# Kernel tuning notes

Hardware: AMD Instinct MI355X
Metric: run time of the kernel (lower is better)

## Reference

```python
import jax, jax.numpy as jnp
import numpy as np

B, U, D, SKIP = 2048, 1024, 1024, 24

def setup_inputs() -> dict:
    key = jax.random.key(0)
    ks = jax.random.split(key, 8)
    return {
        "inputs": jax.random.normal(ks[0], (B, D), dtype=jnp.float32),
        "h_tm1": jax.random.normal(ks[1], (B, 4 * U), dtype=jnp.float32),
        "c_tm1": jax.random.normal(ks[2], (B, U), dtype=jnp.float32),
        "step": jnp.zeros((B, 1), dtype=jnp.float32),
        "prev_h": jax.random.normal(ks[3], (B, U * SKIP), dtype=jnp.float32),
        "kernel": jax.random.normal(ks[4], (D, 4 * U), dtype=jnp.float32) * (1.0 / np.sqrt(D)),
        "recurrent_kernel": jax.random.normal(ks[5], (U, 4 * U), dtype=jnp.float32) * (1.0 / np.sqrt(U)),
        "kernel2": jax.random.normal(ks[6], (U, U), dtype=jnp.float32) * (1.0 / np.sqrt(U)),
        "bias": jnp.zeros((4 * U,), dtype=jnp.float32),
        "bias2": jnp.zeros((U,), dtype=jnp.float32),
        "s0": jnp.float32(0.5),
    }

def reference(inputs, h_tm1, c_tm1, step, prev_h, kernel, recurrent_kernel, kernel2, bias, bias2, s0):
    units = kernel2.shape[0]
    # split previous 'h' state into its four gate-history blocks [B, U] each
    h_parts = jnp.stack(jnp.split(h_tm1, 4, axis=1), axis=0)          # [4, B, U]
    rk = recurrent_kernel.reshape(units, 4, units)                     # [U, 4, U]
    # fused per-gate recurrent matmuls: r[g] = h_parts[g] @ recurrent_kernel[:, g*U:(g+1)*U]
    r = jnp.einsum('gbu,ugv->gbv', h_parts, rk)                        # [4, B, U]
    x = inputs @ kernel + bias                                         # [B, 4U]
    x_i, x_f, x_c, x_o = jnp.split(x, 4, axis=1)
    i = jax.nn.sigmoid(x_i + r[0])
    f = jax.nn.sigmoid(x_f + r[1])
    c = f * c_tm1 + i * jnp.tanh(x_c + r[2])
    o = jax.nn.sigmoid(x_o + r[3])
    h = o * jnp.tanh(c)
    new_h_skip = jax.nn.sigmoid(prev_h[:, :units] @ kernel2 + bias2)
    h = s0 * h + new_h_skip * (1 - s0)
    new_h_tm1 = jnp.concatenate([i, f, c, o], axis=1)
    new_prev_h = jnp.concatenate([prev_h[:, units:], h], axis=1)
    return (h, new_h_tm1, c, step + 1, new_prev_h)
```

## Files before the change

### kernel.cpp

```cpp
#include <hip/hip_runtime.h>
#include <hip/hip_bf16.h>
#include <stdint.h>

#define BB 2048
#define UU 1024
#define SKIPN 24

typedef __attribute__((ext_vector_type(8))) short short8;
typedef __attribute__((ext_vector_type(4))) float f32x4;
typedef __attribute__((ext_vector_type(4))) unsigned short ushort4_t;

static __device__ __forceinline__ float sigmoidf_(float x) {
    return 1.0f / (1.0f + __expf(-x));
}

static __device__ __forceinline__ void load_lds16(const void* g, void* l) {
    __builtin_amdgcn_global_load_lds((const __attribute__((address_space(1))) void*)g,
                                     (__attribute__((address_space(3))) void*)l, 16, 0, 0);
}

static __device__ __forceinline__ f32x4 ntl(const f32x4* p) {
    return __builtin_nontemporal_load(p);
}
static __device__ __forceinline__ void nts(f32x4* p, f32x4 v) {
    __builtin_nontemporal_store(v, p);
}

__global__ __launch_bounds__(256) void prep(
    const float* __restrict__ inputs, const float* __restrict__ h_tm1,
    const float* __restrict__ prev_h, const float* __restrict__ kernel,
    const float* __restrict__ rkernel, const float* __restrict__ kernel2,
    __hip_bfloat16* __restrict__ kt, __hip_bfloat16* __restrict__ rkt,
    __hip_bfloat16* __restrict__ k2t, __hip_bfloat16* __restrict__ xin,
    __hip_bfloat16* __restrict__ hb, __hip_bfloat16* __restrict__ ph0) {
    const int bid = blockIdx.x;
    if (bid < 9216) {
        __shared__ float tile[32][33];
        const float* src;
        __hip_bfloat16* dst;
        int C, local;
        if (bid < 4096)      { src = kernel;  dst = kt;  C = 4096; local = bid; }
        else if (bid < 8192) { src = rkernel; dst = rkt; C = 4096; local = bid - 4096; }
        else                 { src = kernel2; dst = k2t; C = 1024; local = bid - 8192; }
        const int xt = (C == 4096) ? 128 : 32;
        const int bc = (local % xt) * 32;
        const int br = (local / xt) * 32;
        const int tx = threadIdx.x & 31, ty = threadIdx.x >> 5;
#pragma unroll
        for (int i = 0; i < 32; i += 8)
            tile[ty + i][tx] = src[(size_t)(br + ty + i) * C + bc + tx];
        __syncthreads();
#pragma unroll
        for (int i = 0; i < 32; i += 8)
            dst[(size_t)(bc + ty + i) * 1024 + br + tx] = __float2bfloat16(tile[tx][ty + i]);
    } else {
        const int idx = (bid - 9216) * 256 + threadIdx.x;
        const float* src;
        __hip_bfloat16* dst;
        int off;
        if (idx < 524288) { dst = xin; off = idx; src = inputs + (size_t)off * 4; }
        else if (idx < 2621440) { off = idx - 524288; dst = hb; src = h_tm1 + (size_t)off * 4; }
        else {
            const int i = idx - 2621440;
            const int b = i >> 8, c4 = i & 255;
            off = i; dst = ph0;
            src = prev_h + (size_t)b * (UU * SKIPN) + c4 * 4;
        }
        const float4 v = *(const float4*)src;
        union { __hip_bfloat16 h[4]; ushort4_t u; } cv;
        cv.h[0] = __float2bfloat16(v.x);
        cv.h[1] = __float2bfloat16(v.y);
        cv.h[2] = __float2bfloat16(v.z);
        cv.h[3] = __float2bfloat16(v.w);
        *(ushort4_t*)(dst + (size_t)off * 4) = cv.u;
    }
}

__global__ __launch_bounds__(256) void mega4(
    const __hip_bfloat16* __restrict__ xin,
    const __hip_bfloat16* __restrict__ hb,
    const __hip_bfloat16* __restrict__ ph0,
    const __hip_bfloat16* __restrict__ kt,
    const __hip_bfloat16* __restrict__ rkt,
    const __hip_bfloat16* __restrict__ k2t,
    const float* __restrict__ prev_h, float* __restrict__ out_prev,
    float* __restrict__ pre) {
    const int bid = blockIdx.x;
    if (bid >= 640) {
        const int b = bid - 640;
        const f32x4* s = (const f32x4*)(prev_h + (size_t)b * 24576 + 1024);
        f32x4* d = (f32x4*)(out_prev + (size_t)b * 24576);
        int c = threadIdx.x;
#pragma unroll 1
        for (int it = 0; it < 5; ++it) {
            f32x4 v0 = ntl(s + c);
            f32x4 v1 = ntl(s + c + 256);
            f32x4 v2 = ntl(s + c + 512);
            f32x4 v3 = ntl(s + c + 768);
            nts(d + c, v0);
            nts(d + c + 256, v1);
            nts(d + c + 512, v2);
            nts(d + c + 768, v3);
            c += 1024;
        }
        {
            f32x4 v0 = ntl(s + c);
            f32x4 v1 = ntl(s + c + 256);
            f32x4 v2 = ntl(s + c + 512);
            nts(d + c, v0);
            nts(d + c + 256, v1);
            nts(d + c + 512, v2);
        }
        return;
    }
    const int gi = bid;
    const int g = gi % 5;
    const int t = gi / 5;
    const int v0 = (t & 7) * 128;
    const int b0 = (t >> 3) * 128;

    __shared__ char As[2 * 8192];
    __shared__ char Bs[2 * 8192];

    const int tid = threadIdx.x;
    const int lane = tid & 63;
    const int wid = tid >> 6;
    const int wrow = wid >> 1;
    const int wcol = wid & 1;

    const int srow = tid >> 2;
    const int sslot = tid & 3;
    const int kofs = ((sslot ^ (srow & 3)) << 3);
    const int ldst = wid * 1024;

    const int l15 = lane & 15;
    const int hi = lane >> 4;
    const int rswB = ((hi ^ (l15 & 3)) << 4);

    f32x4 acc[4][4];
#pragma unroll
    for (int m = 0; m < 4; m++)
#pragma unroll
        for (int n = 0; n < 4; n++) acc[m][n] = (f32x4){0.f, 0.f, 0.f, 0.f};

    const __hip_bfloat16* A1;
    const __hip_bfloat16* W1;
    const __hip_bfloat16* A2 = nullptr;
    const __hip_bfloat16* W2 = nullptr;
    int lda1;
    if (g < 4) {
        A1 = xin; lda1 = 1024;
        W1 = kt + (size_t)g * 1048576;
        A2 = hb + (size_t)g * 1024;
        W2 = rkt + (size_t)g * 1048576;
    } else {
        A1 = ph0; lda1 = 1024;
        W1 = k2t;
    }

#define BARRIER() asm volatile("s_barrier" ::: "memory")
#define WAITV(N) asm volatile("s_waitcnt vmcnt(" #N ")" ::: "memory")
#define WAITL0() asm volatile("s_waitcnt lgkmcnt(0)" ::: "memory")

#define KSEG(AB, LDA, WB)                                                          \
    {                                                                              \
        const __hip_bfloat16* Ar0 = (AB) + (size_t)(b0 + srow) * (LDA) + kofs;     \
        const __hip_bfloat16* Ar1 = (AB) + (size_t)(b0 + 64 + srow) * (LDA) + kofs;\
        const __hip_bfloat16* Wr0 = (WB) + (size_t)(v0 + srow) * 1024 + kofs;      \
        const __hip_bfloat16* Wr1 = (WB) + (size_t)(v0 + 64 + srow) * 1024 + kofs; \
        load_lds16(Ar0, As + ldst);                                                \
        load_lds16(Ar1, As + ldst + 4096);                                         \
        load_lds16(Wr0, Bs + ldst);                                                \
        load_lds16(Wr1, Bs + ldst + 4096);                                         \
        _Pragma("unroll 2")                                                        \
        for (int t_ = 0; t_ < 32; ++t_) {                                          \
            const int cur = t_ & 1;                                                \
            char* Ac = As + cur * 8192;                                            \
            char* Bc = Bs + cur * 8192;                                            \
            if (t_ < 31) {                                                         \
                const int kn = (t_ + 1) * 32;                                      \
                char* An = As + (cur ^ 1) * 8192 + ldst;                           \
                char* Bn = Bs + (cur ^ 1) * 8192 + ldst;                           \
                load_lds16(Ar0 + kn, An);                                          \
                load_lds16(Ar1 + kn, An + 4096);                                   \
                load_lds16(Wr0 + kn, Bn);                                          \
                load_lds16(Wr1 + kn, Bn + 4096);                                   \
                WAITV(4);                                                          \
            } else {                                                               \
                WAITV(0);                                                          \
            }                                                                      \
            BARRIER();                                                             \
            short8 af[4], bfr[4];                                                  \
            _Pragma("unroll")                                                      \
            for (int m = 0; m < 4; m++)                                            \
                af[m] = *(const short8*)(Ac + (wrow * 64 + m * 16 + l15) * 64 + rswB); \
            _Pragma("unroll")                                                      \
            for (int n = 0; n < 4; n++)                                            \
                bfr[n] = *(const short8*)(Bc + (wcol * 64 + n * 16 + l15) * 64 + rswB); \
            _Pragma("unroll")                                                      \
            for (int m = 0; m < 4; m++)                                            \
                _Pragma("unroll")                                                  \
                for (int n = 0; n < 4; n++)                                        \
                    acc[m][n] = __builtin_amdgcn_mfma_f32_16x16x32_bf16(af[m], bfr[n], acc[m][n], 0, 0, 0); \
            WAITL0();                                                              \
            BARRIER();                                                             \
        }                                                                          \
    }

    KSEG(A1, lda1, W1);
    if (g < 4) KSEG(A2, 4096, W2);
#undef KSEG

    float* P = pre + (size_t)g * 2097152;
#pragma unroll
    for (int m = 0; m < 4; m++) {
#pragma unroll
        for (int n = 0; n < 4; n++) {
            const int col = v0 + wcol * 64 + n * 16 + l15;
            const int row = b0 + wrow * 64 + m * 16 + hi * 4;
#pragma unroll
            for (int r = 0; r < 4; r++)
                P[(size_t)(row + r) * 1024 + col] = acc[m][n][r];
        }
    }
#undef BARRIER
#undef WAITV
#undef WAITL0
}

__global__ __launch_bounds__(256) void epilogue2(
    const float* __restrict__ pre,
    const float* __restrict__ c_tm1, const float* __restrict__ bias,
    const float* __restrict__ bias2, const float* __restrict__ s0p,
    const float* __restrict__ step, float* __restrict__ out_h,
    float* __restrict__ out_ht, float* __restrict__ out_c,
    float* __restrict__ out_step, float* __restrict__ out_prev, int write_tail) {
    const int idx = blockIdx.x * 256 + threadIdx.x;
    const int b = idx >> 8;
    const int v = (idx & 255) * 4;
    const size_t bv = (size_t)b * 1024 + v;
    const float4 pi = *(const float4*)(pre + bv);
    const float4 pf = *(const float4*)(pre + 2097152 + bv);
    const float4 pc = *(const float4*)(pre + 4194304 + bv);
    const float4 po = *(const float4*)(pre + 6291456 + bv);
    const float4 ps = *(const float4*)(pre + 8388608 + bv);
    const float4 ct = *(const float4*)(c_tm1 + bv);
    const float4 bi = *(const float4*)(bias + v);
    const float4 bf_ = *(const float4*)(bias + 1024 + v);
    const float4 bc = *(const float4*)(bias + 2048 + v);
    const float4 bo = *(const float4*)(bias + 3072 + v);
    const float4 b2 = *(const float4*)(bias2 + v);
    const float s0 = s0p[0];

    float4 hv, iv4, fv4, cn4, ov4;
#pragma unroll
    for (int j = 0; j < 4; j++) {
        const float iv = sigmoidf_(((const float*)&pi)[j] + ((const float*)&bi)[j]);
        const float fv = sigmoidf_(((const float*)&pf)[j] + ((const float*)&bf_)[j]);
        const float cn = fv * ((const float*)&ct)[j] + iv * tanhf(((const float*)&pc)[j] + ((const float*)&bc)[j]);
        const float ov = sigmoidf_(((const float*)&po)[j] + ((const float*)&bo)[j]);
        const float sk = sigmoidf_(((const float*)&ps)[j] + ((const float*)&b2)[j]);
        ((float*)&hv)[j] = s0 * (ov * tanhf(cn)) + sk * (1.0f - s0);
        ((float*)&iv4)[j] = iv;
        ((float*)&fv4)[j] = fv;
        ((float*)&cn4)[j] = cn;
        ((float*)&ov4)[j] = ov;
    }
    *(float4*)(out_h + bv) = hv;
    *(float4*)(out_c + bv) = cn4;
    float* ht = out_ht + (size_t)b * 4096 + v;
    *(float4*)(ht) = iv4;
    *(float4*)(ht + 1024) = fv4;
    *(float4*)(ht + 2048) = cn4;
    *(float4*)(ht + 3072) = ov4;
    if (write_tail)
        *(float4*)(out_prev + (size_t)b * 24576 + 23552 + v) = hv;
    if (idx < 2048) out_step[idx] = step[idx] + 1.0f;
}

__global__ __launch_bounds__(256) void shift_only(
    const float* __restrict__ prev_h, const float* __restrict__ out_h,
    float* __restrict__ out_prev) {
    const int b = blockIdx.x;
    float4* d = (float4*)(out_prev + (size_t)b * 24576);
    const float4* s1 = (const float4*)(prev_h + (size_t)b * 24576 + 1024);
    const float4* s2 = (const float4*)(out_h + (size_t)b * 1024);
    for (int c = threadIdx.x; c < 6144; c += 256)
        d[c] = (c < 5888) ? s1[c] : s2[c - 5888];
}

extern "C" void kernel_launch(void* const* d_in, const int* in_sizes, int n_in,
                              void* d_out, int out_size, void* d_ws, size_t ws_size,
                              hipStream_t stream) {
    (void)in_sizes; (void)n_in; (void)out_size;
    const float* inputs = (const float*)d_in[0];
    const float* h_tm1 = (const float*)d_in[1];
    const float* c_tm1 = (const float*)d_in[2];
    const float* step = (const float*)d_in[3];
    const float* prev_h = (const float*)d_in[4];
    const float* kernel = (const float*)d_in[5];
    const float* rkernel = (const float*)d_in[6];
    const float* kernel2 = (const float*)d_in[7];
    const float* bias = (const float*)d_in[8];
    const float* bias2 = (const float*)d_in[9];
    const float* s0 = (const float*)d_in[10];

    float* out = (float*)d_out;
    float* out_h = out;
    float* out_ht = out + 2097152;
    float* out_c = out + 10485760;
    float* out_step = out + 12582912;
    float* out_prev = out + 12584960;

    const size_t NEED = 44040192 + 41943040;
    const int fits = (ws_size >= NEED);
    char* scr = fits ? (char*)d_ws : (char*)out_prev;
    __hip_bfloat16* kt = (__hip_bfloat16*)(scr + 0);
    __hip_bfloat16* rkt = (__hip_bfloat16*)(scr + 8388608);
    __hip_bfloat16* k2t = (__hip_bfloat16*)(scr + 16777216);
    __hip_bfloat16* xin = (__hip_bfloat16*)(scr + 18874368);
    __hip_bfloat16* hb = (__hip_bfloat16*)(scr + 23068672);
    __hip_bfloat16* ph0 = (__hip_bfloat16*)(scr + 39845888);
    float* pre = (float*)(scr + 44040192);

    prep<<<21504, 256, 0, stream>>>(inputs, h_tm1, prev_h, kernel, rkernel, kernel2,
                                    kt, rkt, k2t, xin, hb, ph0);
    if (fits) {
        mega4<<<2688, 256, 0, stream>>>(xin, hb, ph0, kt, rkt, k2t, prev_h, out_prev, pre);
        epilogue2<<<2048, 256, 0, stream>>>(pre, c_tm1, bias, bias2, s0, step,
                                            out_h, out_ht, out_c, out_step, out_prev, 1);
    } else {
        mega4<<<640, 256, 0, stream>>>(xin, hb, ph0, kt, rkt, k2t, prev_h, out_prev, pre);
        epilogue2<<<2048, 256, 0, stream>>>(pre, c_tm1, bias, bias2, s0, step,
                                            out_h, out_ht, out_c, out_step, out_prev, 0);
        shift_only<<<2048, 256, 0, stream>>>(prev_h, out_h, out_prev);
    }
}
```

Baseline: 173.8 us.

## Triple-buffer GEMM LDS pipeline and store preactivations in bf16

Moves the GEMM k-loop from double to triple buffering in LDS, prefetching two k-tiles ahead to hide more global-load latency. Stores the intermediate preactivation buffer as bf16 instead of fp32, halving its write and read traffic and the workspace requirement. The epilogue is reworked to handle 8 elements per thread with half as many blocks. The bf16 rounding of preactivations adds precision loss, and the extra LDS per block may reduce occupancy.

```diff
diff --git a/kernel.cpp b/kernel.cpp
--- a/kernel.cpp
+++ b/kernel.cpp
@@ -76,7 +76,7 @@
     }
 }
 
-__global__ __launch_bounds__(256) void mega4(
+__global__ __launch_bounds__(256) void mega5(
     const __hip_bfloat16* __restrict__ xin,
     const __hip_bfloat16* __restrict__ hb,
     const __hip_bfloat16* __restrict__ ph0,
@@ -84,7 +84,7 @@
     const __hip_bfloat16* __restrict__ rkt,
     const __hip_bfloat16* __restrict__ k2t,
     const float* __restrict__ prev_h, float* __restrict__ out_prev,
-    float* __restrict__ pre) {
+    __hip_bfloat16* __restrict__ pre) {
     const int bid = blockIdx.x;
     if (bid >= 640) {
         const int b = bid - 640;
@@ -119,8 +119,8 @@
     const int v0 = (t & 7) * 128;
     const int b0 = (t >> 3) * 128;
 
-    __shared__ char As[2 * 8192];
-    __shared__ char Bs[2 * 8192];
+    __shared__ char As[3 * 8192];
+    __shared__ char Bs[3 * 8192];
 
     const int tid = threadIdx.x;
     const int lane = tid & 63;
@@ -172,19 +172,25 @@
         load_lds16(Ar1, As + ldst + 4096);                                         \
         load_lds16(Wr0, Bs + ldst);                                                \
         load_lds16(Wr1, Bs + ldst + 4096);                                         \
-        _Pragma("unroll 2")                                                        \
+        load_lds16(Ar0 + 32, As + 8192 + ldst);                                    \
+        load_lds16(Ar1 + 32, As + 8192 + ldst + 4096);                             \
+        load_lds16(Wr0 + 32, Bs + 8192 + ldst);                                    \
+        load_lds16(Wr1 + 32, Bs + 8192 + ldst + 4096);                             \
+        int cur = 0;                                                               \
         for (int t_ = 0; t_ < 32; ++t_) {                                          \
-            const int cur = t_ & 1;                                                \
             char* Ac = As + cur * 8192;                                            \
             char* Bc = Bs + cur * 8192;                                            \
-            if (t_ < 31) {                                                         \
-                const int kn = (t_ + 1) * 32;                                      \
-                char* An = As + (cur ^ 1) * 8192 + ldst;                           \
-                char* Bn = Bs + (cur ^ 1) * 8192 + ldst;                           \
+            if (t_ < 30) {                                                         \
+                int nxt = cur + 2; if (nxt >= 3) nxt -= 3;                         \
+                const int kn = (t_ + 2) * 32;                                      \
+                char* An = As + nxt * 8192 + ldst;                                 \
+                char* Bn = Bs + nxt * 8192 + ldst;                                 \
                 load_lds16(Ar0 + kn, An);                                          \
                 load_lds16(Ar1 + kn, An + 4096);                                   \
                 load_lds16(Wr0 + kn, Bn);                                          \
                 load_lds16(Wr1 + kn, Bn + 4096);                                   \
+                WAITV(8);                                                          \
+            } else if (t_ == 30) {                                                 \
                 WAITV(4);                                                          \
             } else {                                                               \
                 WAITV(0);                                                          \
@@ -204,6 +210,7 @@
                     acc[m][n] = __builtin_amdgcn_mfma_f32_16x16x32_bf16(af[m], bfr[n], acc[m][n], 0, 0, 0); \
             WAITL0();                                                              \
             BARRIER();                                                             \
+            cur = (cur == 2) ? 0 : cur + 1;                                        \
         }                                                                          \
     }
 
@@ -211,7 +218,7 @@
     if (g < 4) KSEG(A2, 4096, W2);
 #undef KSEG
 
-    float* P = pre + (size_t)g * 2097152;
+    __hip_bfloat16* P = pre + (size_t)g * 2097152;
 #pragma unroll
     for (int m = 0; m < 4; m++) {
 #pragma unroll
@@ -220,7 +227,7 @@
             const int row = b0 + wrow * 64 + m * 16 + hi * 4;
 #pragma unroll
             for (int r = 0; r < 4; r++)
-                P[(size_t)(row + r) * 1024 + col] = acc[m][n][r];
+                P[(size_t)(row + r) * 1024 + col] = __float2bfloat16(acc[m][n][r]);
         }
     }
 #undef BARRIER
@@ -228,53 +235,61 @@
 #undef WAITL0
 }
 
-__global__ __launch_bounds__(256) void epilogue2(
-    const float* __restrict__ pre,
+__global__ __launch_bounds__(256) void epilogue3(
+    const __hip_bfloat16* __restrict__ pre,
     const float* __restrict__ c_tm1, const float* __restrict__ bias,
     const float* __restrict__ bias2, const float* __restrict__ s0p,
     const float* __restrict__ step, float* __restrict__ out_h,
     float* __restrict__ out_ht, float* __restrict__ out_c,
     float* __restrict__ out_step, float* __restrict__ out_prev, int write_tail) {
     const int idx = blockIdx.x * 256 + threadIdx.x;
-    const int b = idx >> 8;
-    const int v = (idx & 255) * 4;
+    const int b = idx >> 7;
+    const int v = (idx & 127) * 8;
     const size_t bv = (size_t)b * 1024 + v;
-    const float4 pi = *(const float4*)(pre + bv);
-    const float4 pf = *(const float4*)(pre + 2097152 + bv);
-    const float4 pc = *(const float4*)(pre + 4194304 + bv);
-    const float4 po = *(const float4*)(pre + 6291456 + bv);
-    const float4 ps = *(const float4*)(pre + 8388608 + bv);
-    const float4 ct = *(const float4*)(c_tm1 + bv);
-    const float4 bi = *(const float4*)(bias + v);
-    const float4 bf_ = *(const float4*)(bias + 1024 + v);
-    const float4 bc = *(const float4*)(bias + 2048 + v);
-    const float4 bo = *(const float4*)(bias + 3072 + v);
-    const float4 b2 = *(const float4*)(bias2 + v);
+
+    union u8 { short8 s; unsigned short u[8]; };
+    u8 pi, pf, pc, po, ps;
+    pi.s = *(const short8*)(pre + bv);
+    pf.s = *(const short8*)(pre + 2097152 + bv);
+    pc.s = *(const short8*)(pre + 4194304 + bv);
+    po.s = *(const short8*)(pre + 6291456 + bv);
+    ps.s = *(const short8*)(pre + 8388608 + bv);
     const float s0 = s0p[0];
 
-    float4 hv, iv4, fv4, cn4, ov4;
+    float hv[8], iv8[8], fv8[8], cn8[8], ov8[8];
 #pragma unroll
     for (int j = 0; j < 4; j++) {
-        const float iv = sigmoidf_(((const float*)&pi)[j] + ((const float*)&bi)[j]);
-        const float fv = sigmoidf_(((const float*)&pf)[j] + ((const float*)&bf_)[j]);
-        const float cn = fv * ((const float*)&ct)[j] + iv * tanhf(((const float*)&pc)[j] + ((const float*)&bc)[j]);
-        const float ov = sigmoidf_(((const float*)&po)[j] + ((const float*)&bo)[j]);
-        const float sk = sigmoidf_(((const float*)&ps)[j] + ((const float*)&b2)[j]);
-        ((float*)&hv)[j] = s0 * (ov * tanhf(cn)) + sk * (1.0f - s0);
-        ((float*)&iv4)[j] = iv;
-        ((float*)&fv4)[j] = fv;
-        ((float*)&cn4)[j] = cn;
-        ((float*)&ov4)[j] = ov;
-    }
-    *(float4*)(out_h + bv) = hv;
-    *(float4*)(out_c + bv) = cn4;
-    float* ht = out_ht + (size_t)b * 4096 + v;
-    *(float4*)(ht) = iv4;
-    *(float4*)(ht + 1024) = fv4;
-    *(float4*)(ht + 2048) = cn4;
-    *(float4*)(ht + 3072) = ov4;
-    if (write_tail)
-        *(float4*)(out_prev + (size_t)b * 24576 + 23552 + v) = hv;
+    }
+#pragma unroll
+    for (int j = 0; j < 8; j++) {
+        const float pif = __bfloat162float(*(const __hip_bfloat16*)&pi.u[j]) + bias[v + j];
+        const float pff = __bfloat162float(*(const __hip_bfloat16*)&pf.u[j]) + bias[1024 + v + j];
+        const float pcf = __bfloat162float(*(const __hip_bfloat16*)&pc.u[j]) + bias[2048 + v + j];
+        const float pof = __bfloat162float(*(const __hip_bfloat16*)&po.u[j]) + bias[3072 + v + j];
+        const float psf = __bfloat162float(*(const __hip_bfloat16*)&ps.u[j]) + bias2[v + j];
+        const float ct = c_tm1[bv + j];
+        const float iv = sigmoidf_(pif);
+        const float fv = sigmoidf_(pff);
+        const float cn = fv * ct + iv * tanhf(pcf);
+        const float ov = sigmoidf_(pof);
+        const float sk = sigmoidf_(psf);
+        hv[j] = s0 * (ov * tanhf(cn)) + sk * (1.0f - s0);
+        iv8[j] = iv; fv8[j] = fv; cn8[j] = cn; ov8[j] = ov;
+    }
+#pragma unroll
+    for (int q = 0; q < 2; q++) {
+        const int o = q * 4;
+        *(float4*)(out_h + bv + o) = make_float4(hv[o], hv[o+1], hv[o+2], hv[o+3]);
+        *(float4*)(out_c + bv + o) = make_float4(cn8[o], cn8[o+1], cn8[o+2], cn8[o+3]);
+        float* ht = out_ht + (size_t)b * 4096 + v + o;
+        *(float4*)(ht) = make_float4(iv8[o], iv8[o+1], iv8[o+2], iv8[o+3]);
+        *(float4*)(ht + 1024) = make_float4(fv8[o], fv8[o+1], fv8[o+2], fv8[o+3]);
+        *(float4*)(ht + 2048) = make_float4(cn8[o], cn8[o+1], cn8[o+2], cn8[o+3]);
+        *(float4*)(ht + 3072) = make_float4(ov8[o], ov8[o+1], ov8[o+2], ov8[o+3]);
+        if (write_tail)
+            *(float4*)(out_prev + (size_t)b * 24576 + 23552 + v + o) =
+                make_float4(hv[o], hv[o+1], hv[o+2], hv[o+3]);
+    }
     if (idx < 2048) out_step[idx] = step[idx] + 1.0f;
 }
 
@@ -312,7 +327,7 @@
     float* out_step = out + 12582912;
     float* out_prev = out + 12584960;
 
-    const size_t NEED = 44040192 + 41943040;
+    const size_t NEED = 44040192 + 20971520;
     const int fits = (ws_size >= NEED);
     char* scr = fits ? (char*)d_ws : (char*)out_prev;
     __hip_bfloat16* kt = (__hip_bfloat16*)(scr + 0);
@@ -321,17 +336,17 @@
     __hip_bfloat16* xin = (__hip_bfloat16*)(scr + 18874368);
     __hip_bfloat16* hb = (__hip_bfloat16*)(scr + 23068672);
     __hip_bfloat16* ph0 = (__hip_bfloat16*)(scr + 39845888);
-    float* pre = (float*)(scr + 44040192);
+    __hip_bfloat16* pre = (__hip_bfloat16*)(scr + 44040192);
 
     prep<<<21504, 256, 0, stream>>>(inputs, h_tm1, prev_h, kernel, rkernel, kernel2,
                                     kt, rkt, k2t, xin, hb, ph0);
     if (fits) {
-        mega4<<<2688, 256, 0, stream>>>(xin, hb, ph0, kt, rkt, k2t, prev_h, out_prev, pre);
-        epilogue2<<<2048, 256, 0, stream>>>(pre, c_tm1, bias, bias2, s0, step,
+        mega5<<<2688, 256, 0, stream>>>(xin, hb, ph0, kt, rkt, k2t, prev_h, out_prev, pre);
+        epilogue3<<<1024, 256, 0, stream>>>(pre, c_tm1, bias, bias2, s0, step,
                                             out_h, out_ht, out_c, out_step, out_prev, 1);
     } else {
-        mega4<<<640, 256, 0, stream>>>(xin, hb, ph0, kt, rkt, k2t, prev_h, out_prev, pre);
-        epilogue2<<<2048, 256, 0, stream>>>(pre, c_tm1, bias, bias2, s0, step,
+        mega5<<<640, 256, 0, stream>>>(xin, hb, ph0, kt, rkt, k2t, prev_h, out_prev, pre);
+        epilogue3<<<1024, 256, 0, stream>>>(pre, c_tm1, bias, bias2, s0, step,
                                             out_h, out_ht, out_c, out_step, out_prev, 0);
         shift_only<<<2048, 256, 0, stream>>>(prev_h, out_h, out_prev);
     }
```

Result: faster. 161.7 us (-7.0%).
